# Optimization experiments

Measured on AMD Instinct MI355X. Metric: run time of the kernel, lower is better.

The kernel has to match this reference:

```python
import jax, jax.numpy as jnp
import numpy as np

C = 256
GROUPS = 32
EPS = 1e-5


def setup_inputs() -> dict:
    key = jax.random.key(0)
    ks = jax.random.split(key, 6)
    b, c, H, W = 8, C, 64, 64
    s = 1.0 / np.sqrt(c)
    return {
        "x": jax.random.normal(ks[0], (b, c, H, W), dtype=jnp.float32),
        "gn_scale": jnp.ones((c,), jnp.float32),
        "gn_bias": jnp.zeros((c,), jnp.float32),
        "wq": jax.random.normal(ks[1], (c, c), jnp.float32) * s,
        "bq": jnp.zeros((c,), jnp.float32),
        "wk": jax.random.normal(ks[2], (c, c), jnp.float32) * s,
        "bk": jnp.zeros((c,), jnp.float32),
        "wv": jax.random.normal(ks[3], (c, c), jnp.float32) * s,
        "bv": jnp.zeros((c,), jnp.float32),
        "wo": jax.random.normal(ks[4], (c, c), jnp.float32) * s,
        "bo": jnp.zeros((c,), jnp.float32),
    }


def reference(x, gn_scale, gn_bias, wq, bq, wk, bk, wv, bv, wo, bo):
    b, c, H, W = x.shape
    N = H * W
    # GroupNorm(32, c)
    xg = x.reshape(b, GROUPS, c // GROUPS, H, W)
    mean = xg.mean(axis=(2, 3, 4), keepdims=True)
    var = xg.var(axis=(2, 3, 4), keepdims=True)
    xn = ((xg - mean) * jax.lax.rsqrt(var + EPS)).reshape(b, c, H, W)
    xn = xn * gn_scale[None, :, None, None] + gn_bias[None, :, None, None]
    xf = xn.reshape(b, c, N)  # [b, c, N]
    # 1x1 convs == per-pixel channel matmuls
    q = jnp.einsum('oc,bcn->bon', wq, xf) + bq[None, :, None]
    k = jnp.einsum('oc,bcn->bon', wk, xf) + bk[None, :, None]
    v = jnp.einsum('oc,bcn->bon', wv, xf) + bv[None, :, None]
    # attention: scores [b, N, N]
    scale = 1.0 / jnp.sqrt(jnp.asarray(c, x.dtype))
    w = jnp.einsum('bcn,bcm->bnm', q, k) * scale
    w = jax.nn.softmax(w, axis=-1)
    attn = jnp.einsum('bnm,bcm->bcn', w, v)  # [b, c, N]
    out = jnp.einsum('oc,bcn->bon', wo, attn) + bo[None, :, None]
    return x + out.reshape(b, c, H, W)
```

## Files before the change

### kernel.cpp

```cpp
#include <hip/hip_runtime.h>

typedef __attribute__((ext_vector_type(8))) short short8;
typedef __attribute__((ext_vector_type(4))) float floatx4;
typedef __attribute__((ext_vector_type(16))) float floatx16;
typedef __attribute__((ext_vector_type(4))) int intx4;

#define NPIX 4096
#define CH 256

static __device__ __forceinline__ unsigned short f2bf(float f) {
  union { float f; unsigned int u; } v; v.f = f;
  unsigned int u = v.u;
  return (unsigned short)((u + 0x7FFFu + ((u >> 16) & 1u)) >> 16);
}

static __device__ __forceinline__ unsigned int pk2bf(float a, float b) {
  union { float f; unsigned int u; } x, y; x.f = a; y.f = b;
  return __builtin_amdgcn_perm(y.u + 0x8000u, x.u + 0x8000u, 0x07060302u);
}

typedef __attribute__((address_space(3))) unsigned int lds_uint;
typedef const __attribute__((address_space(1))) unsigned int glob_uint;
static __device__ __forceinline__ void gload16(const void* g, void* l) {
  __builtin_amdgcn_global_load_lds((glob_uint*)g, (lds_uint*)l, 16, 0, 0);
}

__global__ void conv_weights_kernel(const float* __restrict__ wq, const float* __restrict__ wk,
                                    const float* __restrict__ wv, const float* __restrict__ wo,
                                    unsigned short* __restrict__ wqkv, unsigned short* __restrict__ wob) {
  int i = blockIdx.x * 256 + threadIdx.x;
  wqkv[i]          = f2bf(wq[i]);
  wqkv[65536 + i]  = f2bf(wk[i]);
  wqkv[131072 + i] = f2bf(wv[i]);
  wob[i]           = f2bf(wo[i]);
}

__global__ __launch_bounds__(256) void gn_kernel(const float* __restrict__ x,
                                                 const float* __restrict__ gsc,
                                                 const float* __restrict__ gbi,
                                                 unsigned short* __restrict__ xnT) {
  int blk = blockIdx.x; int b = blk >> 5; int g = blk & 31;
  int c0 = g * 8;
  const float* xb = x + ((size_t)b * CH + c0) * NPIX;
  int tid = threadIdx.x;
  float s = 0.f, ss = 0.f;
#pragma unroll
  for (int ci = 0; ci < 8; ++ci) {
    const floatx4* p = (const floatx4*)(xb + (size_t)ci * NPIX);
    for (int n4 = tid; n4 < 1024; n4 += 256) {
      floatx4 v = p[n4];
      s += v[0] + v[1] + v[2] + v[3];
      ss += v[0]*v[0] + v[1]*v[1] + v[2]*v[2] + v[3]*v[3];
    }
  }
#pragma unroll
  for (int o = 32; o > 0; o >>= 1) { s += __shfl_down(s, o); ss += __shfl_down(ss, o); }
  __shared__ float red[10];
  int wid = tid >> 6;
  if ((tid & 63) == 0) { red[wid] = s; red[4 + wid] = ss; }
  __syncthreads();
  if (tid == 0) {
    float S = red[0] + red[1] + red[2] + red[3];
    float SS = red[4] + red[5] + red[6] + red[7];
    float mean = S * (1.f / 32768.f);
    float var = SS * (1.f / 32768.f) - mean * mean;
    red[8] = mean; red[9] = rsqrtf(var + 1e-5f);
  }
  __syncthreads();
  float mean = red[8], rstd = red[9];
  float sc[8], bi[8];
#pragma unroll
  for (int ci = 0; ci < 8; ++ci) {
    float scale = gsc[c0 + ci] * rstd;
    sc[ci] = scale;
    bi[ci] = gbi[c0 + ci] - mean * scale;
  }
  for (int n4 = tid; n4 < 1024; n4 += 256) {
    floatx4 v[8];
#pragma unroll
    for (int ci = 0; ci < 8; ++ci) v[ci] = ((const floatx4*)(xb + (size_t)ci * NPIX))[n4];
#pragma unroll
    for (int j = 0; j < 4; ++j) {
      alignas(16) unsigned short tmp[8];
#pragma unroll
      for (int ci = 0; ci < 8; ++ci) tmp[ci] = f2bf(v[ci][j] * sc[ci] + bi[ci]);
      *(intx4*)(xnT + ((size_t)(b * NPIX + n4 * 4 + j)) * CH + c0) = *(const intx4*)tmp;
    }
  }
}

__global__ __launch_bounds__(256, 2) void qkv_gemm(
    const unsigned short* __restrict__ wqkv, const unsigned short* __restrict__ xnT,
    const float* __restrict__ bq, const float* __restrict__ bk, const float* __restrict__ bv,
    unsigned short* __restrict__ qT, unsigned short* __restrict__ kT, unsigned short* __restrict__ vC) {
  int nt = blockIdx.x, ot = blockIdx.y, bz = blockIdx.z;
  int which = bz % 3, b = bz / 3;
  const unsigned short* W = wqkv + which * 65536;
  const float* bias = which == 0 ? bq : (which == 1 ? bk : bv);
  const unsigned short* X = xnT + (size_t)b * NPIX * CH;
  int o0 = ot * 128, n0 = nt * 128;

  __shared__ unsigned short As[128 * 64];
  __shared__ unsigned short Bs[128 * 64];

  int tid = threadIdx.x;
  int wave = tid >> 6, lane = tid & 63, quad = lane >> 4, l16 = lane & 15;
  int wm = (wave >> 1) * 64, wn = (wave & 1) * 64;

  floatx4 acc[4][4];
#pragma unroll
  for (int i = 0; i < 4; ++i)
#pragma unroll
    for (int j = 0; j < 4; ++j) acc[i][j] = (floatx4){0.f, 0.f, 0.f, 0.f};

  for (int k0 = 0; k0 < 256; k0 += 64) {
    __syncthreads();
#pragma unroll
    for (int c2 = 0; c2 < 4; ++c2) {
      int row = wave * 32 + c2 * 8 + (lane >> 3);
      int sc = (lane & 7) ^ (row & 7);
      gload16(W + (size_t)(o0 + row) * CH + k0 + sc * 8, &As[(wave * 32 + c2 * 8) * 64]);
      gload16(X + (size_t)(n0 + row) * CH + k0 + sc * 8, &Bs[(wave * 32 + c2 * 8) * 64]);
    }
    __syncthreads();
#pragma unroll
    for (int s = 0; s < 2; ++s) {
      short8 af[4], bf[4];
#pragma unroll
      for (int i = 0; i < 4; ++i) {
        int m = wm + i * 16 + l16;
        af[i] = *(const short8*)(As + m * 64 + (((s * 4 + quad) ^ (m & 7)) * 8));
        int n = wn + i * 16 + l16;
        bf[i] = *(const short8*)(Bs + n * 64 + (((s * 4 + quad) ^ (n & 7)) * 8));
      }
#pragma unroll
      for (int i = 0; i < 4; ++i)
#pragma unroll
        for (int j = 0; j < 4; ++j)
          acc[i][j] = __builtin_amdgcn_mfma_f32_16x16x32_bf16(af[i], bf[j], acc[i][j], 0, 0, 0);
    }
  }

  if (which < 2) {
    float qs = (which == 0) ? 0.090168440f : 1.0f;
    unsigned short* outp = (which == 0 ? qT : kT) + (size_t)b * NPIX * CH;
#pragma unroll
    for (int i = 0; i < 4; ++i) {
      int obase = o0 + wm + i * 16 + quad * 4;
      float bias4[4];
#pragma unroll
      for (int r = 0; r < 4; ++r) bias4[r] = bias[obase + r];
#pragma unroll
      for (int j = 0; j < 4; ++j) {
        int n = n0 + wn + j * 16 + l16;
        uint2 pk;
        pk.x = pk2bf((acc[i][j][0] + bias4[0]) * qs, (acc[i][j][1] + bias4[1]) * qs);
        pk.y = pk2bf((acc[i][j][2] + bias4[2]) * qs, (acc[i][j][3] + bias4[3]) * qs);
        *(uint2*)(outp + (size_t)n * CH + obase) = pk;
      }
    }
  } else {
    unsigned short* outp = vC + (size_t)b * CH * NPIX;
#pragma unroll
    for (int i = 0; i < 4; ++i)
#pragma unroll
      for (int r = 0; r < 4; ++r) {
        int o = o0 + wm + i * 16 + quad * 4 + r;
        float bb = bias[o];
#pragma unroll
        for (int j = 0; j < 4; ++j) {
          int n = n0 + wn + j * 16 + l16;
          outp[(size_t)o * NPIX + n] = f2bf(acc[i][j][r] + bb);
        }
      }
  }
}

__global__ __launch_bounds__(512, 2) void attn_kernel(
    const unsigned short* __restrict__ qT, const unsigned short* __restrict__ kT,
    const unsigned short* __restrict__ vC, unsigned short* __restrict__ aT) {
  __shared__ unsigned short Klds[128 * 256];
  __shared__ unsigned short Vlds[256 * 128];
  __shared__ unsigned short Plds[128 * 128];

  const int tid = threadIdx.x;
  const int w = tid >> 6, lane = tid & 63;
  const int l32 = lane & 31, h = lane >> 5;
  const int b = blockIdx.x & 7, qt = blockIdx.x >> 3;
  const int qbase = qt * 128;

  const unsigned short* Kb = kT + (size_t)b * NPIX * CH;
  const unsigned short* Vb = vC + (size_t)b * CH * NPIX;

  const int mp  = (w & 1) * 64;
  const int qsl = (w >> 1) * 32;
  const int csl = (w & 3) * 64;
  const int qp  = (w >> 2) * 64;

  short8 qf[16];
  {
    const unsigned short* qq = qT + ((size_t)(b * NPIX + qbase + qsl + l32)) * CH + h * 8;
#pragma unroll
    for (int ks = 0; ks < 16; ++ks) qf[ks] = *(const short8*)(qq + ks * 16);
  }

  floatx16 o00 = {}, o01 = {}, o10 = {}, o11 = {};
  float l_acc = 0.f;

#define STAGE_K(KT)                                                              \
  {                                                                              \
    int m0_ = (KT) * 128;                                                        \
    _Pragma("unroll") for (int j = 0; j < 8; ++j) {                              \
      int r_ = w * 16 + j * 2 + h;                                               \
      gload16(Kb + (size_t)(m0_ + r_) * CH + ((l32 ^ (r_ & 31)) * 8),            \
              &Klds[(w * 16 + j * 2) * 256]);                                    \
    }                                                                            \
  }
#define STAGE_V(KT)                                                              \
  {                                                                              \
    int m0_ = (KT) * 128;                                                        \
    _Pragma("unroll") for (int j = 0; j < 8; ++j) {                              \
      int c_ = w * 32 + j * 4 + (lane >> 4);                                     \
      gload16(Vb + (size_t)c_ * NPIX + m0_ + (((lane & 15) ^ (c_ & 15)) * 8),    \
              &Vlds[(w * 32 + j * 4) * 128]);                                    \
    }                                                                            \
  }

  STAGE_K(0);
  asm volatile("s_waitcnt vmcnt(0)\ns_barrier" ::: "memory");

  for (int kt = 0; kt < 32; ++kt) {
    STAGE_V(kt);

    floatx16 s0 = {}, s1 = {};
    {
      const unsigned short* kr0 = &Klds[(mp + l32) * 256];
      const unsigned short* kr1 = &Klds[(mp + 32 + l32) * 256];
      const int mx = l32;
#pragma unroll
      for (int ks = 0; ks < 16; ++ks) {
        int off = ((ks * 2 + h) ^ mx) * 8;
        short8 kf0 = *(const short8*)(kr0 + off);
        short8 kf1 = *(const short8*)(kr1 + off);
        s0 = __builtin_amdgcn_mfma_f32_32x32x16_bf16(kf0, qf[ks], s0, 0, 0, 0);
        s1 = __builtin_amdgcn_mfma_f32_32x32x16_bf16(kf1, qf[ks], s1, 0, 0, 0);
      }
    }
    float sum = 0.f;
#pragma unroll
    for (int r = 0; r < 16; ++r) {
      float p0 = exp2f(s0[r]); s0[r] = p0; sum += p0;
      float p1 = exp2f(s1[r]); s1[r] = p1; sum += p1;
    }
    sum += __shfl_xor(sum, 32);
    l_acc += sum;

    {
      int qrow = qsl + l32;
      int qx = qrow & 15;
      char* Pq = (char*)Plds + qrow * 256 + h * 8;
      int g0 = (w & 1) * 8;
#pragma unroll
      for (int t = 0; t < 4; ++t) {
        uint2 wv;
        wv.x = pk2bf(s0[4 * t], s0[4 * t + 1]);
        wv.y = pk2bf(s0[4 * t + 2], s0[4 * t + 3]);
        *(uint2*)(Pq + (((g0 + t) ^ qx) * 16)) = wv;
        wv.x = pk2bf(s1[4 * t], s1[4 * t + 1]);
        wv.y = pk2bf(s1[4 * t + 2], s1[4 * t + 3]);
        *(uint2*)(Pq + (((g0 + 4 + t) ^ qx) * 16)) = wv;
      }
    }
    asm volatile("s_waitcnt vmcnt(0) lgkmcnt(0)\ns_barrier" ::: "memory");
    if (kt + 1 < 32) STAGE_K(kt + 1);

    {
      const int q0 = qp + l32, q1 = qp + 32 + l32;
      const int c0 = csl + l32, c1 = csl + 32 + l32;
      const char* Pb = (const char*)Plds;
      const char* Vl = (const char*)Vlds;
#pragma unroll
      for (int ks = 0; ks < 8; ++ks) {
        int sl = ks * 2 + h;
        short8 pf0 = *(const short8*)(Pb + q0 * 256 + ((sl ^ (q0 & 15)) * 16));
        short8 pf1 = *(const short8*)(Pb + q1 * 256 + ((sl ^ (q1 & 15)) * 16));
        short8 vf0 = *(const short8*)(Vl + c0 * 256 + ((sl ^ (c0 & 15)) * 16));
        short8 vf1 = *(const short8*)(Vl + c1 * 256 + ((sl ^ (c1 & 15)) * 16));
        o00 = __builtin_amdgcn_mfma_f32_32x32x16_bf16(vf0, pf0, o00, 0, 0, 0);
        o01 = __builtin_amdgcn_mfma_f32_32x32x16_bf16(vf0, pf1, o01, 0, 0, 0);
        o10 = __builtin_amdgcn_mfma_f32_32x32x16_bf16(vf1, pf0, o10, 0, 0, 0);
        o11 = __builtin_amdgcn_mfma_f32_32x32x16_bf16(vf1, pf1, o11, 0, 0, 0);
      }
    }
    asm volatile("s_waitcnt vmcnt(0) lgkmcnt(0)\ns_barrier" ::: "memory");
  }
#undef STAGE_K
#undef STAGE_V

  float* lred = (float*)Plds;
  if (lane < 32) lred[(qsl + l32) * 2 + (w & 1)] = l_acc;
  __syncthreads();
  float inv0, inv1;
  {
    const float* lp0 = &lred[(qp + l32) * 2];
    inv0 = 1.f / (lp0[0] + lp0[1]);
    const float* lp1 = &lred[(qp + 32 + l32) * 2];
    inv1 = 1.f / (lp1[0] + lp1[1]);
  }

  unsigned short* ab = aT + (size_t)b * NPIX * CH;
#define STORE_TILE(OO, CSUB, QSUB, IV)                                           \
  {                                                                              \
    int qg = qbase + qp + (QSUB) * 32 + l32;                                     \
    _Pragma("unroll") for (int t = 0; t < 4; ++t) {                              \
      int c = csl + (CSUB) * 32 + 8 * t + 4 * h;                                 \
      uint2 wv;                                                                  \
      wv.x = pk2bf(OO[4 * t] * (IV), OO[4 * t + 1] * (IV));                      \
      wv.y = pk2bf(OO[4 * t + 2] * (IV), OO[4 * t + 3] * (IV));                  \
      *(uint2*)(ab + (size_t)qg * CH + c) = wv;                                  \
    }                                                                            \
  }
  STORE_TILE(o00, 0, 0, inv0)
  STORE_TILE(o01, 0, 1, inv1)
  STORE_TILE(o10, 1, 0, inv0)
  STORE_TILE(o11, 1, 1, inv1)
#undef STORE_TILE
}

__global__ __launch_bounds__(256, 2) void out_gemm(
    const unsigned short* __restrict__ wob, const unsigned short* __restrict__ aT,
    const float* __restrict__ bo, const float* __restrict__ x, float* __restrict__ outp) {
  int nt = blockIdx.x, ot = blockIdx.y, b = blockIdx.z;
  const unsigned short* A = aT + (size_t)b * NPIX * CH;
  int o0 = ot * 128, n0 = nt * 128;

  __shared__ unsigned short As[128 * 64];
  __shared__ unsigned short Bs[128 * 64];

  int tid = threadIdx.x;
  int wave = tid >> 6, lane = tid & 63, quad = lane >> 4, l16 = lane & 15;
  int wm = (wave >> 1) * 64, wn = (wave & 1) * 64;

  floatx4 acc[4][4];
#pragma unroll
  for (int i = 0; i < 4; ++i)
#pragma unroll
    for (int j = 0; j < 4; ++j) acc[i][j] = (floatx4){0.f, 0.f, 0.f, 0.f};

  for (int k0 = 0; k0 < 256; k0 += 64) {
    __syncthreads();
#pragma unroll
    for (int c2 = 0; c2 < 4; ++c2) {
      int row = wave * 32 + c2 * 8 + (lane >> 3);
      int sc = (lane & 7) ^ (row & 7);
      gload16(wob + (size_t)(o0 + row) * CH + k0 + sc * 8, &As[(wave * 32 + c2 * 8) * 64]);
      gload16(A + (size_t)(n0 + row) * CH + k0 + sc * 8, &Bs[(wave * 32 + c2 * 8) * 64]);
    }
    __syncthreads();
#pragma unroll
    for (int s = 0; s < 2; ++s) {
      short8 af[4], bf[4];
#pragma unroll
      for (int i = 0; i < 4; ++i) {
        int m = wm + i * 16 + l16;
        af[i] = *(const short8*)(As + m * 64 + (((s * 4 + quad) ^ (m & 7)) * 8));
        int n = wn + i * 16 + l16;
        bf[i] = *(const short8*)(Bs + n * 64 + (((s * 4 + quad) ^ (n & 7)) * 8));
      }
#pragma unroll
      for (int i = 0; i < 4; ++i)
#pragma unroll
        for (int j = 0; j < 4; ++j)
          acc[i][j] = __builtin_amdgcn_mfma_f32_16x16x32_bf16(af[i], bf[j], acc[i][j], 0, 0, 0);
    }
  }

#pragma unroll
  for (int i = 0; i < 4; ++i)
#pragma unroll
    for (int r = 0; r < 4; ++r) {
      int o = o0 + wm + i * 16 + quad * 4 + r;
      float bb = bo[o];
#pragma unroll
      for (int j = 0; j < 4; ++j) {
        int n = n0 + wn + j * 16 + l16;
        size_t idx = ((size_t)b * CH + o) * NPIX + n;
        outp[idx] = x[idx] + bb + acc[i][j][r];
      }
    }
}

extern "C" void kernel_launch(void* const* d_in, const int* in_sizes, int n_in,
                              void* d_out, int out_size, void* d_ws, size_t ws_size,
                              hipStream_t stream) {
  const float* x   = (const float*)d_in[0];
  const float* gsc = (const float*)d_in[1];
  const float* gbi = (const float*)d_in[2];
  const float* wq  = (const float*)d_in[3];
  const float* bq  = (const float*)d_in[4];
  const float* wk  = (const float*)d_in[5];
  const float* bk  = (const float*)d_in[6];
  const float* wv  = (const float*)d_in[7];
  const float* bv  = (const float*)d_in[8];
  const float* wo  = (const float*)d_in[9];
  const float* bo  = (const float*)d_in[10];
  float* out = (float*)d_out;

  char* ws = (char*)d_ws;
  unsigned short* xnT  = (unsigned short*)(ws);
  unsigned short* qT   = (unsigned short*)(ws + 16777216);
  unsigned short* kT   = (unsigned short*)(ws + 33554432);
  unsigned short* vC   = (unsigned short*)(ws + 50331648);
  unsigned short* wqkv = (unsigned short*)(ws + 67108864);
  unsigned short* wob  = (unsigned short*)(ws + 67502080);
  unsigned short* aT   = (unsigned short*)(ws + 67633152);

  conv_weights_kernel<<<256, 256, 0, stream>>>(wq, wk, wv, wo, wqkv, wob);
  gn_kernel<<<256, 256, 0, stream>>>(x, gsc, gbi, xnT);
  dim3 g1(32, 2, 24);
  qkv_gemm<<<g1, 256, 0, stream>>>(wqkv, xnT, bq, bk, bv, qT, kT, vC);
  attn_kernel<<<256, 512, 0, stream>>>(qT, kT, vC, aT);
  dim3 g3(32, 2, 8);
  out_gemm<<<g3, 256, 0, stream>>>(wob, aT, bo, x, out);
}
```

Before: 343.9 us.

## Double-buffer K tiles in LDS and read V fragments directly from global

The V tile is no longer staged through LDS. Each wave now loads its V fragments straight from global memory inside the PV loop, and the freed LDS holds a second K buffer. The next K tile is prefetched at the top of each iteration, so its load overlaps the QK and PV compute, and the mid-iteration vmcnt wait is dropped. The trade-off is that V is re-read from global/L2 by several waves per block without LDS sharing, and those loads sit on the critical path of the PV MFMAs.

After: 420.1 us. +22.2%, slower.

```diff
diff --git a/kernel.cpp b/kernel.cpp
--- a/kernel.cpp
+++ b/kernel.cpp
@@ -179,8 +179,7 @@
 __global__ __launch_bounds__(512, 2) void attn_kernel(
     const unsigned short* __restrict__ qT, const unsigned short* __restrict__ kT,
     const unsigned short* __restrict__ vC, unsigned short* __restrict__ aT) {
-  __shared__ unsigned short Klds[128 * 256];
-  __shared__ unsigned short Vlds[256 * 128];
+  __shared__ unsigned short Klds[2][128 * 256];
   __shared__ unsigned short Plds[128 * 128];
 
   const int tid = threadIdx.x;
@@ -204,38 +203,33 @@
     for (int ks = 0; ks < 16; ++ks) qf[ks] = *(const short8*)(qq + ks * 16);
   }
 
+  const unsigned short* vrow0 = Vb + (size_t)(csl + l32) * NPIX;
+  const unsigned short* vrow1 = Vb + (size_t)(csl + 32 + l32) * NPIX;
+
   floatx16 o00 = {}, o01 = {}, o10 = {}, o11 = {};
   float l_acc = 0.f;
 
-#define STAGE_K(KT)                                                              \
+#define STAGE_K(KT, BUF)                                                         \
   {                                                                              \
     int m0_ = (KT) * 128;                                                        \
     _Pragma("unroll") for (int j = 0; j < 8; ++j) {                              \
       int r_ = w * 16 + j * 2 + h;                                               \
       gload16(Kb + (size_t)(m0_ + r_) * CH + ((l32 ^ (r_ & 31)) * 8),            \
-              &Klds[(w * 16 + j * 2) * 256]);                                    \
+              &Klds[BUF][(w * 16 + j * 2) * 256]);                               \
     }                                                                            \
   }
-#define STAGE_V(KT)                                                              \
-  {                                                                              \
-    int m0_ = (KT) * 128;                                                        \
-    _Pragma("unroll") for (int j = 0; j < 8; ++j) {                              \
-      int c_ = w * 32 + j * 4 + (lane >> 4);                                     \
-      gload16(Vb + (size_t)c_ * NPIX + m0_ + (((lane & 15) ^ (c_ & 15)) * 8),    \
-              &Vlds[(w * 32 + j * 4) * 128]);                                    \
-    }                                                                            \
-  }
-
-  STAGE_K(0);
+
+  STAGE_K(0, 0);
   asm volatile("s_waitcnt vmcnt(0)\ns_barrier" ::: "memory");
 
   for (int kt = 0; kt < 32; ++kt) {
-    STAGE_V(kt);
+    const int buf = kt & 1;
+    if (kt + 1 < 32) STAGE_K(kt + 1, buf ^ 1);
 
     floatx16 s0 = {}, s1 = {};
     {
-      const unsigned short* kr0 = &Klds[(mp + l32) * 256];
-      const unsigned short* kr1 = &Klds[(mp + 32 + l32) * 256];
+      const unsigned short* kr0 = &Klds[buf][(mp + l32) * 256];
+      const unsigned short* kr1 = &Klds[buf][(mp + 32 + l32) * 256];
       const int mx = l32;
 #pragma unroll
       for (int ks = 0; ks < 16; ++ks) {
@@ -271,21 +265,20 @@
         *(uint2*)(Pq + (((g0 + 4 + t) ^ qx) * 16)) = wv;
       }
     }
-    asm volatile("s_waitcnt vmcnt(0) lgkmcnt(0)\ns_barrier" ::: "memory");
-    if (kt + 1 < 32) STAGE_K(kt + 1);
+    asm volatile("s_waitcnt lgkmcnt(0)\ns_barrier" ::: "memory");
 
     {
       const int q0 = qp + l32, q1 = qp + 32 + l32;
-      const int c0 = csl + l32, c1 = csl + 32 + l32;
       const char* Pb = (const char*)Plds;
-      const char* Vl = (const char*)Vlds;
+      const unsigned short* v0p = vrow0 + kt * 128;
+      const unsigned short* v1p = vrow1 + kt * 128;
 #pragma unroll
       for (int ks = 0; ks < 8; ++ks) {
         int sl = ks * 2 + h;
+        short8 vf0 = *(const short8*)(v0p + sl * 8);
+        short8 vf1 = *(const short8*)(v1p + sl * 8);
         short8 pf0 = *(const short8*)(Pb + q0 * 256 + ((sl ^ (q0 & 15)) * 16));
         short8 pf1 = *(const short8*)(Pb + q1 * 256 + ((sl ^ (q1 & 15)) * 16));
-        short8 vf0 = *(const short8*)(Vl + c0 * 256 + ((sl ^ (c0 & 15)) * 16));
-        short8 vf1 = *(const short8*)(Vl + c1 * 256 + ((sl ^ (c1 & 15)) * 16));
         o00 = __builtin_amdgcn_mfma_f32_32x32x16_bf16(vf0, pf0, o00, 0, 0, 0);
         o01 = __builtin_amdgcn_mfma_f32_32x32x16_bf16(vf0, pf1, o01, 0, 0, 0);
         o10 = __builtin_amdgcn_mfma_f32_32x32x16_bf16(vf1, pf0, o10, 0, 0, 0);
@@ -295,7 +288,6 @@
     asm volatile("s_waitcnt vmcnt(0) lgkmcnt(0)\ns_barrier" ::: "memory");
   }
 #undef STAGE_K
-#undef STAGE_V
 
   float* lred = (float*)Plds;
   if (lane < 32) lred[(qsl + l32) * 2 + (w & 1)] = l_acc;
```
